# Kernel optimization log

Hardware: AMD Instinct MI355X
Metric: run time of the kernel (lower is better)

## Reference

```python
import math
import jax
import jax.numpy as jnp
import numpy as np

T, B, C, F = 4096, 8, 1024, 128


def setup_inputs() -> dict:
    key = jax.random.key(0)
    ks = jax.random.split(key, 16)
    sc = 0.02
    inp = {
        "x": jax.random.normal(ks[0], (T, B, C), jnp.float32),
        "state": jax.random.normal(ks[1], (B, F, F), jnp.float32),
        "A_w": jax.random.normal(ks[2], (F, C), jnp.float32) * sc,
        "A_b": jax.random.normal(ks[3], (F,), jnp.float32) * sc,
        "B_w": jax.random.normal(ks[4], (F, C), jnp.float32) * sc,
        "B_b": jax.random.normal(ks[5], (F,), jnp.float32) * sc,
        "C_w": jax.random.normal(ks[6], (F, C), jnp.float32) * sc,
        "C_b": jax.random.normal(ks[7], (F,), jnp.float32) * sc,
        "D_w": jax.random.normal(ks[8], (F, C), jnp.float32) * sc,
        "D_b": jax.random.normal(ks[9], (F,), jnp.float32) * sc,
        "I_w": jax.random.normal(ks[10], (F, C), jnp.float32) * sc,
        "I_b": jax.random.normal(ks[11], (F,), jnp.float32) * sc,
        "S_w": jax.random.normal(ks[12], (F, C), jnp.float32) * sc,
        "S_b": jax.random.normal(ks[13], (F,), jnp.float32) * sc,
        "O_w": jax.random.normal(ks[14], (C, F), jnp.float32) * sc,
    }
    return inp


def reference(x, state, A_w, A_b, B_w, B_b, C_w, C_b, D_w, D_b, I_w, I_b, S_w, S_b, O_w):
    # x: [T, B, C], state: [B, F, F]
    awk_safe = jnp.asarray(math.sqrt(F), x.dtype)

    def proj(W, b):
        return jnp.einsum('tbc,fc->tbf', x, W) + b  # [T, B, F]

    a = proj(A_w, A_b)
    b = proj(B_w, B_b)
    c = proj(C_w, C_b)
    d = proj(D_w, D_b)
    i = proj(I_w, I_b)
    s = proj(S_w, S_b)

    def step(st, ins):
        sel, at, bt, ct, dt, it = ins  # each [B, F]
        # st: [B, F, F]
        st = (st * jax.nn.sigmoid(it)[:, None, :]
              + jnp.einsum('bij,bj->bi', st, at)[:, :, None] * bt[:, None, :] / awk_safe
              + ct[:, :, None] * dt[:, None, :])
        out = jnp.einsum('bi,bij->bj', sel, st)  # [B, F]
        return st, out

    state_out, o = jax.lax.scan(step, state, (s, a, b, c, d, i))
    y = jnp.einsum('tbf,cf->tbc', o, O_w)  # O has no bias
    return y, state_out
```

## Files before the change

### kernel.cpp

```cpp
#include <hip/hip_runtime.h>


#define T_DIM 4096
#define B_DIM 8
#define C_DIM 1024
#define F_DIM 128

typedef __attribute__((ext_vector_type(8))) short bf16x8;
typedef __attribute__((ext_vector_type(4))) float f32x4;

__device__ __forceinline__ unsigned short f2bf(float f) {
  unsigned u = __float_as_uint(f);
  u += 0x7fffu + ((u >> 16) & 1u);
  return (unsigned short)(u >> 16);
}
__device__ __forceinline__ float bfu2f(unsigned u) { return __uint_as_float(u << 16); }

__global__ void cvt_kernel(const float* __restrict__ in, unsigned short* __restrict__ out, int n4) {
  int i = blockIdx.x * blockDim.x + threadIdx.x;
  int stride = gridDim.x * blockDim.x;
  for (; i < n4; i += stride) {
    float4 v = ((const float4*)in)[i];
    ushort4 r;
    r.x = f2bf(v.x); r.y = f2bf(v.y); r.z = f2bf(v.z); r.w = f2bf(v.w);
    ((ushort4*)out)[i] = r;
  }
}

__global__ void pack_w_kernel(const float* __restrict__ Aw, const float* __restrict__ Ab,
                              const float* __restrict__ Bw, const float* __restrict__ Bb,
                              const float* __restrict__ Cw, const float* __restrict__ Cb,
                              const float* __restrict__ Dw, const float* __restrict__ Db,
                              const float* __restrict__ Iw, const float* __restrict__ Ib,
                              const float* __restrict__ Sw, const float* __restrict__ Sb,
                              unsigned short* __restrict__ Wall, float* __restrict__ biasAll) {
  const float scaleB = 0.08838834764831845f;
  int idx = blockIdx.x * 256 + threadIdx.x;
  if (idx < 768 * 1024) {
    int row = idx >> 10, c = idx & 1023;
    int slot = row >> 7, rr = row & 127;
    const float* W = slot == 0 ? Aw : slot == 1 ? Bw : slot == 2 ? Cw
                   : slot == 3 ? Dw : slot == 4 ? Iw : Sw;
    float v = W[rr * 1024 + c];
    if (slot == 1) v *= scaleB;
    Wall[idx] = f2bf(v);
  }
  if (idx < 768) {
    int slot = idx >> 7, rr = idx & 127;
    const float* Bv = slot == 0 ? Ab : slot == 1 ? Bb : slot == 2 ? Cb
                    : slot == 3 ? Db : slot == 4 ? Ib : Sb;
    float v = Bv[rr];
    if (slot == 1) v *= scaleB;
    biasAll[idx] = v;
  }
}

__global__ __launch_bounds__(256) void gemm_bt(
    const unsigned short* __restrict__ A,
    const unsigned short* __restrict__ Bm,
    float* __restrict__ Cm,
    const float* __restrict__ bias,
    int M, int N, int K, int sig_lo, int sig_hi) {
  __shared__ unsigned short As[128 * 32];
  __shared__ unsigned short Bs[128 * 32];
  const int tid = threadIdx.x;
  const int m0 = blockIdx.x * 128;
  const int n0 = blockIdx.y * 128;
  const int wv = tid >> 6, ln = tid & 63;
  const int mo = (wv & 1) * 64, no = (wv >> 1) * 64;
  const int lrow = ln & 15, lq = ln >> 4;
  f32x4 acc[4][4] = {};

  for (int kt = 0; kt < K; kt += 32) {
#pragma unroll
    for (int it = 0; it < 2; ++it) {
      int idx = it * 256 + tid;
      int row = idx >> 2, kc = idx & 3;
      *(int4*)&As[row * 32 + kc * 8] = *(const int4*)&A[(size_t)(m0 + row) * K + kt + kc * 8];
      *(int4*)&Bs[row * 32 + kc * 8] = *(const int4*)&Bm[(size_t)(n0 + row) * K + kt + kc * 8];
    }
    __syncthreads();
    bf16x8 af[4], bf[4];
#pragma unroll
    for (int i = 0; i < 4; ++i) {
      af[i] = *(const bf16x8*)&As[(mo + i * 16 + lrow) * 32 + lq * 8];
      bf[i] = *(const bf16x8*)&Bs[(no + i * 16 + lrow) * 32 + lq * 8];
    }
#pragma unroll
    for (int i = 0; i < 4; ++i)
#pragma unroll
      for (int j = 0; j < 4; ++j)
        acc[i][j] = __builtin_amdgcn_mfma_f32_16x16x32_bf16(af[i], bf[j], acc[i][j], 0, 0, 0);
    __syncthreads();
  }

#pragma unroll
  for (int i = 0; i < 4; ++i) {
#pragma unroll
    for (int j = 0; j < 4; ++j) {
      int col = n0 + no + j * 16 + lrow;
      float bv = bias ? bias[col] : 0.0f;
      bool sig = (col >= sig_lo) && (col < sig_hi);
#pragma unroll
      for (int r = 0; r < 4; ++r) {
        int row = m0 + mo + i * 16 + lq * 4 + r;
        float v = acc[i][j][r] + bv;
        if (sig) v = 1.0f / (1.0f + __expf(-v));
        Cm[(size_t)row * N + col] = v;
      }
    }
  }
}

__device__ __forceinline__ float wave_sum64(float x) {
  x += __int_as_float(__builtin_amdgcn_update_dpp(0, __float_as_int(x), 0x111, 0xf, 0xf, false));
  x += __int_as_float(__builtin_amdgcn_update_dpp(0, __float_as_int(x), 0x112, 0xf, 0xf, false));
  x += __int_as_float(__builtin_amdgcn_update_dpp(0, __float_as_int(x), 0x114, 0xf, 0xf, false));
  x += __int_as_float(__builtin_amdgcn_update_dpp(0, __float_as_int(x), 0x118, 0xf, 0xf, false));
  x += __int_as_float(__builtin_amdgcn_update_dpp(0, __float_as_int(x), 0x142, 0xf, 0xf, false));
  x += __int_as_float(__builtin_amdgcn_update_dpp(0, __float_as_int(x), 0x143, 0xf, 0xf, false));
  return __int_as_float(__builtin_amdgcn_readlane(__float_as_int(x), 63));
}

template <int ROWS>
__global__ __launch_bounds__(256, 1) void scan_kernel(
    const float* __restrict__ P,
    const float* __restrict__ state_in,
    unsigned short* __restrict__ o_part,
    float* __restrict__ state_out) {
  const int b = blockIdx.x;
  const int gq = blockIdx.y;
  const int wave = threadIdx.x >> 6;
  const int lane = threadIdx.x & 63;
  const int r0 = gq * (4 * ROWS) + wave * ROWS;
  const int j0 = lane * 2;
  __shared__ float buf[2][4][8][128];

  float2 st[ROWS];
#pragma unroll
  for (int r = 0; r < ROWS; ++r)
    st[r] = *(const float2*)&state_in[((size_t)b * F_DIM + r0 + r) * F_DIM + j0];

  float2 Pa[8], Pb[8], Pd[8], Pg[8];
  float Pc[8][ROWS], Ps[8][ROWS];
  const size_t PSTEP = (size_t)B_DIM * 768;
  const float* P0 = P + (size_t)b * 768;

#define RING_LOAD(sl, Pt)                                                   \
  do {                                                                      \
    Pa[sl] = *(const float2*)((Pt) + 0 + j0);                               \
    Pb[sl] = *(const float2*)((Pt) + 128 + j0);                             \
    Pd[sl] = *(const float2*)((Pt) + 384 + j0);                             \
    Pg[sl] = *(const float2*)((Pt) + 512 + j0);                             \
    if constexpr (ROWS == 2) {                                              \
      float2 v_ = *(const float2*)((Pt) + 256 + r0);                        \
      Pc[sl][0] = v_.x; Pc[sl][1] = v_.y;                                   \
      float2 w_ = *(const float2*)((Pt) + 640 + r0);                        \
      Ps[sl][0] = w_.x; Ps[sl][1] = w_.y;                                   \
    } else {                                                                \
      float4 v_ = *(const float4*)((Pt) + 256 + r0);                        \
      Pc[sl][0] = v_.x; Pc[sl][1] = v_.y; Pc[sl][2] = v_.z; Pc[sl][3] = v_.w; \
      float4 w_ = *(const float4*)((Pt) + 640 + r0);                        \
      Ps[sl][0] = w_.x; Ps[sl][1] = w_.y; Ps[sl][2] = w_.z; Ps[sl][3] = w_.w; \
    }                                                                       \
  } while (0)

#pragma unroll
  for (int k = 0; k < 8; ++k) RING_LOAD(k, P0 + (size_t)k * PSTEP);

  for (int t8 = 0; t8 < T_DIM; t8 += 8) {
    const int pb = (t8 >> 3) & 1;
#pragma unroll
    for (int k = 0; k < 8; ++k) {
      float2 a2 = Pa[k], b2 = Pb[k], d2 = Pd[k], g2 = Pg[k];
      float cc[ROWS], ss[ROWS];
#pragma unroll
      for (int r = 0; r < ROWS; ++r) { cc[r] = Pc[k][r]; ss[r] = Ps[k][r]; }

      const float* Pn = P0 + (size_t)(t8 + k + 8) * PSTEP;
      RING_LOAD(k, Pn);

      float vr[ROWS];
#pragma unroll
      for (int r = 0; r < ROWS; ++r)
        vr[r] = wave_sum64(st[r].x * a2.x + st[r].y * a2.y);

      float ox = 0.0f, oy = 0.0f;
#pragma unroll
      for (int r = 0; r < ROWS; ++r) {
        st[r].x = st[r].x * g2.x + vr[r] * b2.x + cc[r] * d2.x;
        st[r].y = st[r].y * g2.y + vr[r] * b2.y + cc[r] * d2.y;
        ox += ss[r] * st[r].x;
        oy += ss[r] * st[r].y;
      }
      *(float2*)&buf[pb][wave][k][j0] = make_float2(ox, oy);
      __builtin_amdgcn_sched_barrier(0);
    }
    asm volatile("s_waitcnt lgkmcnt(0)" ::: "memory");
    __builtin_amdgcn_s_barrier();
    asm volatile("" ::: "memory");

#pragma unroll
    for (int h = 0; h < 2; ++h) {
      int it = threadIdx.x + h * 256;
      int k = it >> 6, c2 = (it & 63) * 2;
      float2 s0 = *(const float2*)&buf[pb][0][k][c2];
      float2 s1 = *(const float2*)&buf[pb][1][k][c2];
      float2 s2 = *(const float2*)&buf[pb][2][k][c2];
      float2 s3 = *(const float2*)&buf[pb][3][k][c2];
      float sx = s0.x + s1.x + s2.x + s3.x;
      float sy = s0.y + s1.y + s2.y + s3.y;
      unsigned pk = (unsigned)f2bf(sx) | ((unsigned)f2bf(sy) << 16);
      *(unsigned*)&o_part[(((size_t)gq * T_DIM + t8 + k) * B_DIM + b) * F_DIM + c2] = pk;
    }
  }
#undef RING_LOAD

#pragma unroll
  for (int r = 0; r < ROWS; ++r)
    *(float2*)&state_out[((size_t)b * F_DIM + r0 + r) * F_DIM + j0] = st[r];
}

__global__ void reduce_kernel(const unsigned short* __restrict__ o_part,
                              unsigned short* __restrict__ ob, int G) {
  const size_t NEL = (size_t)T_DIM * B_DIM * F_DIM;
  size_t i = ((size_t)blockIdx.x * 256 + threadIdx.x) * 8;
  if (i >= NEL) return;
  float acc[8] = {0, 0, 0, 0, 0, 0, 0, 0};
  for (int g = 0; g < G; ++g) {
    int4 v = *(const int4*)(o_part + (size_t)g * NEL + i);
    unsigned w0 = (unsigned)v.x, w1 = (unsigned)v.y, w2 = (unsigned)v.z, w3 = (unsigned)v.w;
    acc[0] += bfu2f(w0 & 0xffffu); acc[1] += bfu2f(w0 >> 16);
    acc[2] += bfu2f(w1 & 0xffffu); acc[3] += bfu2f(w1 >> 16);
    acc[4] += bfu2f(w2 & 0xffffu); acc[5] += bfu2f(w2 >> 16);
    acc[6] += bfu2f(w3 & 0xffffu); acc[7] += bfu2f(w3 >> 16);
  }
  int4 o;
  o.x = (int)((unsigned)f2bf(acc[0]) | ((unsigned)f2bf(acc[1]) << 16));
  o.y = (int)((unsigned)f2bf(acc[2]) | ((unsigned)f2bf(acc[3]) << 16));
  o.z = (int)((unsigned)f2bf(acc[4]) | ((unsigned)f2bf(acc[5]) << 16));
  o.w = (int)((unsigned)f2bf(acc[6]) | ((unsigned)f2bf(acc[7]) << 16));
  *(int4*)(ob + i) = o;
}

extern "C" void kernel_launch(void* const* d_in, const int* in_sizes, int n_in,
                              void* d_out, int out_size, void* d_ws, size_t ws_size,
                              hipStream_t stream) {
  const float* x  = (const float*)d_in[0];
  const float* st = (const float*)d_in[1];
  const float* Aw = (const float*)d_in[2];
  const float* Ab = (const float*)d_in[3];
  const float* Bw = (const float*)d_in[4];
  const float* Bb = (const float*)d_in[5];
  const float* Cw = (const float*)d_in[6];
  const float* Cb = (const float*)d_in[7];
  const float* Dw = (const float*)d_in[8];
  const float* Db = (const float*)d_in[9];
  const float* Iw = (const float*)d_in[10];
  const float* Ib = (const float*)d_in[11];
  const float* Sw = (const float*)d_in[12];
  const float* Sb = (const float*)d_in[13];
  const float* Ow = (const float*)d_in[14];

  float* y = (float*)d_out;
  float* state_out = y + (size_t)T_DIM * B_DIM * C_DIM;

  char* ws = (char*)d_ws;
  unsigned short* Wall = (unsigned short*)(ws);
  float* biasAll       = (float*)(ws + 1572864);
  unsigned short* Owb  = (unsigned short*)(ws + 1576960);
  float* P             = (float*)(ws + 1839104);
  unsigned short* ob   = (unsigned short*)(ws + 102502400);
  unsigned short* xb   = (unsigned short*)(ws + 110891008);
  unsigned short* o_part = xb;

  const int G = (ws_size >= 245108736u) ? 16 : 8;

  cvt_kernel<<<4096, 256, 0, stream>>>(x, xb, 33554432 / 4);
  pack_w_kernel<<<3072, 256, 0, stream>>>(Aw, Ab, Bw, Bb, Cw, Cb, Dw, Db, Iw, Ib, Sw, Sb,
                                          Wall, biasAll);
  cvt_kernel<<<128, 256, 0, stream>>>(Ow, Owb, 131072 / 4);
  gemm_bt<<<dim3(256, 6), 256, 0, stream>>>(xb, Wall, P, biasAll, 32768, 768, 1024, 512, 640);
  if (G == 16)
    scan_kernel<2><<<dim3(8, 16), 256, 0, stream>>>(P, st, o_part, state_out);
  else
    scan_kernel<4><<<dim3(8, 8), 256, 0, stream>>>(P, st, o_part, state_out);
  reduce_kernel<<<2048, 256, 0, stream>>>(o_part, ob, G);
  gemm_bt<<<dim3(256, 8), 256, 0, stream>>>(ob, Owb, y, nullptr, 32768, 1024, 128, 0, 0);
}
```

Measured before the change: 1.272 ms.

## Stage per-step projections into LDS via async global_load_lds double buffering

Replaces the per-thread register ring of global loads for the projected parameters with a block-wide asynchronous global-to-LDS copy. Each batch of 8 timesteps is staged into a double-buffered shared array, and every step then reads its values from LDS with one step of software prefetch. The aim is to cut redundant global traffic, since all waves share the same a/b/d/g vectors, and to reduce register pressure in the serial scan. In exchange it adds LDS reads inside the latency-bound recurrence and a vmcnt wait at every batch barrier. It also leaves stage_batch at the final iteration reading past the end of the T range.

Result: faster. 1.136 ms (-10.7%).

```diff
diff --git a/kernel.cpp b/kernel.cpp
--- a/kernel.cpp
+++ b/kernel.cpp
@@ -15,6 +15,11 @@
   return (unsigned short)(u >> 16);
 }
 __device__ __forceinline__ float bfu2f(unsigned u) { return __uint_as_float(u << 16); }
+
+__device__ __forceinline__ void gload_lds16(const float* g, float* l) {
+  __builtin_amdgcn_global_load_lds((const __attribute__((address_space(1))) void*)g,
+                                   (__attribute__((address_space(3))) void*)l, 16, 0, 0);
+}
 
 __global__ void cvt_kernel(const float* __restrict__ in, unsigned short* __restrict__ out, int n4) {
   int i = blockIdx.x * blockDim.x + threadIdx.x;
@@ -134,6 +139,7 @@
   const int lane = threadIdx.x & 63;
   const int r0 = gq * (4 * ROWS) + wave * ROWS;
   const int j0 = lane * 2;
+  __shared__ float stage[2][8][768];
   __shared__ float buf[2][4][8][128];
 
   float2 st[ROWS];
@@ -141,62 +147,76 @@
   for (int r = 0; r < ROWS; ++r)
     st[r] = *(const float2*)&state_in[((size_t)b * F_DIM + r0 + r) * F_DIM + j0];
 
-  float2 Pa[8], Pb[8], Pd[8], Pg[8];
-  float Pc[8][ROWS], Ps[8][ROWS];
-  const size_t PSTEP = (size_t)B_DIM * 768;
-  const float* P0 = P + (size_t)b * 768;
-
-#define RING_LOAD(sl, Pt)                                                   \
-  do {                                                                      \
-    Pa[sl] = *(const float2*)((Pt) + 0 + j0);                               \
-    Pb[sl] = *(const float2*)((Pt) + 128 + j0);                             \
-    Pd[sl] = *(const float2*)((Pt) + 384 + j0);                             \
-    Pg[sl] = *(const float2*)((Pt) + 512 + j0);                             \
-    if constexpr (ROWS == 2) {                                              \
-      float2 v_ = *(const float2*)((Pt) + 256 + r0);                        \
-      Pc[sl][0] = v_.x; Pc[sl][1] = v_.y;                                   \
-      float2 w_ = *(const float2*)((Pt) + 640 + r0);                        \
-      Ps[sl][0] = w_.x; Ps[sl][1] = w_.y;                                   \
-    } else {                                                                \
-      float4 v_ = *(const float4*)((Pt) + 256 + r0);                        \
-      Pc[sl][0] = v_.x; Pc[sl][1] = v_.y; Pc[sl][2] = v_.z; Pc[sl][3] = v_.w; \
-      float4 w_ = *(const float4*)((Pt) + 640 + r0);                        \
-      Ps[sl][0] = w_.x; Ps[sl][1] = w_.y; Ps[sl][2] = w_.z; Ps[sl][3] = w_.w; \
-    }                                                                       \
+  auto stage_batch = [&](int sb, int tstart) {
+#pragma unroll
+    for (int c6 = 0; c6 < 6; ++c6) {
+      int tl = wave * 2 + (c6 >= 3 ? 1 : 0);
+      int part = c6 - (c6 >= 3 ? 3 : 0);
+      const float* g = P + ((size_t)(tstart + tl) * B_DIM + b) * 768 + part * 256 + lane * 4;
+      gload_lds16(g, &stage[sb][tl][part * 256]);
+    }
+  };
+
+#define LDS_STEP(da, db, dd, dg, dc, ds, sb, kk)                             \
+  do {                                                                       \
+    const float* Sp = &stage[sb][kk][0];                                     \
+    da = *(const float2*)(Sp + 0 + j0);                                      \
+    db = *(const float2*)(Sp + 128 + j0);                                    \
+    dd = *(const float2*)(Sp + 384 + j0);                                    \
+    dg = *(const float2*)(Sp + 512 + j0);                                    \
+    if constexpr (ROWS == 2) {                                               \
+      float2 v_ = *(const float2*)(Sp + 256 + r0);                           \
+      dc[0] = v_.x; dc[1] = v_.y;                                            \
+      float2 w_ = *(const float2*)(Sp + 640 + r0);                           \
+      ds[0] = w_.x; ds[1] = w_.y;                                            \
+    } else {                                                                 \
+      float4 v_ = *(const float4*)(Sp + 256 + r0);                           \
+      dc[0] = v_.x; dc[1] = v_.y; dc[2] = v_.z; dc[3] = v_.w;                \
+      float4 w_ = *(const float4*)(Sp + 640 + r0);                           \
+      ds[0] = w_.x; ds[1] = w_.y; ds[2] = w_.z; ds[3] = w_.w;                \
+    }                                                                        \
   } while (0)
 
-#pragma unroll
-  for (int k = 0; k < 8; ++k) RING_LOAD(k, P0 + (size_t)k * PSTEP);
-
+  stage_batch(0, 0);
+  asm volatile("s_waitcnt vmcnt(0)" ::: "memory");
+  __builtin_amdgcn_s_barrier();
+  asm volatile("" ::: "memory");
+
+  int cur = 0;
   for (int t8 = 0; t8 < T_DIM; t8 += 8) {
     const int pb = (t8 >> 3) & 1;
+    stage_batch(cur ^ 1, t8 + 8);
+
+    float2 a2, b2, d2, g2;
+    float cc[ROWS], ss[ROWS];
+    LDS_STEP(a2, b2, d2, g2, cc, ss, cur, 0);
+
 #pragma unroll
     for (int k = 0; k < 8; ++k) {
-      float2 a2 = Pa[k], b2 = Pb[k], d2 = Pd[k], g2 = Pg[k];
-      float cc[ROWS], ss[ROWS];
-#pragma unroll
-      for (int r = 0; r < ROWS; ++r) { cc[r] = Pc[k][r]; ss[r] = Ps[k][r]; }
-
-      const float* Pn = P0 + (size_t)(t8 + k + 8) * PSTEP;
-      RING_LOAD(k, Pn);
+      float2 ca = a2, cb = b2, cd = d2, cg = g2;
+      float lc[ROWS], ls[ROWS];
+#pragma unroll
+      for (int r = 0; r < ROWS; ++r) { lc[r] = cc[r]; ls[r] = ss[r]; }
+      if (k < 7) LDS_STEP(a2, b2, d2, g2, cc, ss, cur, k + 1);
 
       float vr[ROWS];
 #pragma unroll
       for (int r = 0; r < ROWS; ++r)
-        vr[r] = wave_sum64(st[r].x * a2.x + st[r].y * a2.y);
+        vr[r] = wave_sum64(st[r].x * ca.x + st[r].y * ca.y);
 
       float ox = 0.0f, oy = 0.0f;
 #pragma unroll
       for (int r = 0; r < ROWS; ++r) {
-        st[r].x = st[r].x * g2.x + vr[r] * b2.x + cc[r] * d2.x;
-        st[r].y = st[r].y * g2.y + vr[r] * b2.y + cc[r] * d2.y;
-        ox += ss[r] * st[r].x;
-        oy += ss[r] * st[r].y;
+        st[r].x = st[r].x * cg.x + vr[r] * cb.x + lc[r] * cd.x;
+        st[r].y = st[r].y * cg.y + vr[r] * cb.y + lc[r] * cd.y;
+        ox += ls[r] * st[r].x;
+        oy += ls[r] * st[r].y;
       }
       *(float2*)&buf[pb][wave][k][j0] = make_float2(ox, oy);
       __builtin_amdgcn_sched_barrier(0);
     }
-    asm volatile("s_waitcnt lgkmcnt(0)" ::: "memory");
+
+    asm volatile("s_waitcnt vmcnt(0) lgkmcnt(0)" ::: "memory");
     __builtin_amdgcn_s_barrier();
     asm volatile("" ::: "memory");
 
@@ -213,8 +233,9 @@
       unsigned pk = (unsigned)f2bf(sx) | ((unsigned)f2bf(sy) << 16);
       *(unsigned*)&o_part[(((size_t)gq * T_DIM + t8 + k) * B_DIM + b) * F_DIM + c2] = pk;
     }
-  }
-#undef RING_LOAD
+    cur ^= 1;
+  }
+#undef LDS_STEP
 
 #pragma unroll
   for (int r = 0; r < ROWS; ++r)
```
